# Kernel optimization log

Hardware: AMD Instinct MI355X
Metric: run time of the kernel (lower is better)

Reference implementation:

```python
import jax, jax.numpy as jnp
import numpy as np

KERNEL_SIZE = 9
B, C, H, W = 8, 32, 512, 512


def setup_inputs() -> dict:
    key = jax.random.key(0)
    image = jax.random.uniform(key, (B, C, H, W), dtype=jnp.float32)
    return {"image": image}


def _make_kernels(channels, k, dtype):
    # kernel1: point-select (identity) depthwise kernel
    k1 = jnp.zeros((channels, 1, k, k), dtype=dtype).at[:, 0, k // 2, k // 2].set(1.0)
    # kernel2: all -2, center = k*k - 2
    k2 = jnp.full((channels, 1, k, k), -2.0, dtype=dtype).at[:, 0, k // 2, k // 2].set(float(k * k - 2))
    # kernel3: ones box filter
    k3 = jnp.ones((channels, 1, k, k), dtype=dtype)
    return k1, k2, k3


def _dwconv(x, ker, channels, k):
    pad = k // 2  # 'same' padding for odd k
    return jax.lax.conv_general_dilated(
        x, ker,
        window_strides=(1, 1),
        padding=[(pad, pad), (pad, pad)],
        dimension_numbers=("NCHW", "OIHW", "NCHW"),
        feature_group_count=channels,
    )


def reference(image):
    channels = image.shape[1]
    k = KERNEL_SIZE
    k1, k2, k3 = _make_kernels(channels, k, image.dtype)
    im_sq = jnp.square(image)
    conv1 = _dwconv(image, k1, channels, k)   # identity point-select
    conv2 = _dwconv(image, k2, channels, k)   # box(-2) with center correction
    conv3 = _dwconv(im_sq, k3, channels, k)   # box sum of squares
    convsum = conv1 * conv2 + conv3
    # sum over (C,H,W) per batch element, then mean over batch
    return jnp.mean(jnp.sum(convsum, axis=(1, 2, 3)))
```

## Files before the change

kernel.cpp:

```cpp
#include <hip/hip_runtime.h>

#define HH 512
#define WW 512
#define SEGS 16
#define SEGROWS 32
#define CG 128

__device__ __forceinline__ int imax(int a, int b) { return a > b ? a : b; }
__device__ __forceinline__ int imin(int a, int b) { return a < b ? a : b; }

__global__ __launch_bounds__(256, 4) void scc_kernel(const float* __restrict__ img,
                                                     float* __restrict__ out) {
    const int tid   = blockIdx.x * 256 + threadIdx.x;
    const int g     = tid & (CG - 1);
    const int rest  = tid >> 7;
    const int seg   = rest & (SEGS - 1);
    const int plane = rest >> 4;

    const float* base = img + (size_t)plane * (HH * WW);
    const int r0 = seg * SEGROWS;

    float4 cw;
    {
        int w0 = 4 * g;
        cw.x = (float)(9 - imax(0, 4 - (w0 + 0)) - imax(0, (w0 + 0) - (WW - 5)));
        cw.y = (float)(9 - imax(0, 4 - (w0 + 1)) - imax(0, (w0 + 1) - (WW - 5)));
        cw.z = (float)(9 - imax(0, 4 - (w0 + 2)) - imax(0, (w0 + 2) - (WW - 5)));
        cw.w = (float)(9 - imax(0, 4 - (w0 + 3)) - imax(0, (w0 + 3) - (WW - 5)));
    }

    const int offL = imax(g - 1, 0) * 16;
    const int offC = g * 16;
    const int offR = imin(g + 1, CG - 1) * 16;
    const float mL = (g > 0) ? 1.f : 0.f;
    const float mR = (g < CG - 1) ? 1.f : 0.f;

    const float4 z4 = make_float4(0.f, 0.f, 0.f, 0.f);
    float4 x0 = z4, x1 = z4, x2 = z4, x3 = z4, x4 = z4,
           x5 = z4, x6 = z4, x7 = z4, x8 = z4;
    float4 q0 = z4, q1 = z4, q2 = z4, q3 = z4, q4 = z4;
    float4 V = z4;
    float accW = 0.f, accRV = 0.f;

#pragma unroll 8
    for (int i = 0; i < SEGROWS + 8; ++i) {
        const int r  = r0 - 4 + i;
        const int rc_ = imin(imax(r, 0), HH - 1);
        const float m = ((unsigned)r < (unsigned)HH) ? 1.f : 0.f;
        const char* rowb = (const char*)(base + (ptrdiff_t)rc_ * WW);

        float4 lcr = *(const float4*)(rowb + offL);
        float4 ccr = *(const float4*)(rowb + offC);
        float4 rcr = *(const float4*)(rowb + offR);

        const float a = mL * m, b = mR * m;
        float4 lc = make_float4(lcr.x * a, lcr.y * a, lcr.z * a, lcr.w * a);
        float4 cc = make_float4(ccr.x * m, ccr.y * m, ccr.z * m, ccr.w * m);
        float4 rc = make_float4(rcr.x * b, rcr.y * b, rcr.z * b, rcr.w * b);

        float R0 = ((lc.x + lc.y) + (lc.z + lc.w)) + ((cc.x + cc.y) + (cc.z + cc.w)) + rc.x;
        float R1 = R0 - lc.x + rc.y;
        float R2 = R1 - lc.y + rc.z;
        float R3 = R2 - lc.z + rc.w;
        float4 Rn = make_float4(R0, R1, R2, R3);

        V.x += cc.x - x0.x;  V.y += cc.y - x0.y;
        V.z += cc.z - x0.z;  V.w += cc.w - x0.w;

        x0 = x1; x1 = x2; x2 = x3; x3 = x4; x4 = x5;
        x5 = x6; x6 = x7; x7 = x8; x8 = cc;
        q0 = q1; q1 = q2; q2 = q3; q3 = q4; q4 = Rn;

        if (i >= 8) {
            const int h = r - 4;
            const float chf = (float)(9 - imax(0, 4 - h) - imax(0, h - (HH - 5)));
            float w0 = fmaf(chf, cw.x, 81.f);
            float w1 = fmaf(chf, cw.y, 81.f);
            float w2 = fmaf(chf, cw.z, 81.f);
            float w3 = fmaf(chf, cw.w, 81.f);
            accW = fmaf(w0 * x4.x, x4.x, accW);
            accW = fmaf(w1 * x4.y, x4.y, accW);
            accW = fmaf(w2 * x4.z, x4.z, accW);
            accW = fmaf(w3 * x4.w, x4.w, accW);
            accRV = fmaf(q0.x, V.x, accRV);
            accRV = fmaf(q0.y, V.y, accRV);
            accRV = fmaf(q0.z, V.z, accRV);
            accRV = fmaf(q0.w, V.w, accRV);
        }
    }

    float acc = accW - 2.f * accRV;

#pragma unroll
    for (int off = 32; off > 0; off >>= 1)
        acc += __shfl_xor(acc, off, 64);
    __shared__ float wsum[4];
    const int lane = threadIdx.x & 63;
    const int wv   = threadIdx.x >> 6;
    if (lane == 0) wsum[wv] = acc;
    __syncthreads();
    if (threadIdx.x == 0) {
        float s = (wsum[0] + wsum[1]) + (wsum[2] + wsum[3]);
        atomicAdd(out, 0.125f * s);
    }
}

extern "C" void kernel_launch(void* const* d_in, const int* in_sizes, int n_in,
                              void* d_out, int out_size, void* d_ws, size_t ws_size,
                              hipStream_t stream) {
    const float* img = (const float*)d_in[0];
    float* out = (float*)d_out;
    hipMemsetAsync(out, 0, sizeof(float), stream);
    scc_kernel<<<dim3(2048), dim3(256), 0, stream>>>(img, out);
}
```

Measured before the change: 371.5 us.

## Double segment height, halve grid, swizzle block order, peel warm-up rows

Each thread now streams 64 output rows instead of 32, which halves the grid to 1024 blocks and cuts the redundant 8-row halo reads per segment. Block indices are swizzled so consecutive blocks land on different planes and segments, to spread memory traffic across channels and XCDs. The 8-row warm-up is peeled into a separate unrolled loop, which removes the per-iteration i>=8 branch from the main loop. The trade-off is fewer resident waves on a device with many CUs, which may reduce latency hiding.

```diff
diff --git a/kernel.cpp b/kernel.cpp
--- a/kernel.cpp
+++ b/kernel.cpp
@@ -2,20 +2,50 @@
 
 #define HH 512
 #define WW 512
-#define SEGS 16
-#define SEGROWS 32
+#define SEGS 8
+#define LOG2SEGS 3
+#define SEGROWS 64
 #define CG 128
+#define NBLOCKS 1024
 
 __device__ __forceinline__ int imax(int a, int b) { return a > b ? a : b; }
 __device__ __forceinline__ int imin(int a, int b) { return a < b ? a : b; }
 
+
+#define STREAM_ROW(rr)                                                         \
+    {                                                                          \
+        const int r   = (rr);                                                  \
+        const int rc_ = imin(imax(r, 0), HH - 1);                              \
+        const float m = ((unsigned)r < (unsigned)HH) ? 1.f : 0.f;              \
+        const char* rowb = (const char*)(base + (ptrdiff_t)rc_ * WW);          \
+        float4 lcr = *(const float4*)(rowb + offL);                            \
+        float4 ccr = *(const float4*)(rowb + offC);                            \
+        float4 rcr = *(const float4*)(rowb + offR);                            \
+        const float a = mL * m, b = mR * m;                                    \
+        float4 lc = make_float4(lcr.x * a, lcr.y * a, lcr.z * a, lcr.w * a);   \
+        float4 cc = make_float4(ccr.x * m, ccr.y * m, ccr.z * m, ccr.w * m);   \
+        float4 rc = make_float4(rcr.x * b, rcr.y * b, rcr.z * b, rcr.w * b);   \
+        float R0 = ((lc.x + lc.y) + (lc.z + lc.w)) +                           \
+                   ((cc.x + cc.y) + (cc.z + cc.w)) + rc.x;                     \
+        float R1 = R0 - lc.x + rc.y;                                           \
+        float R2 = R1 - lc.y + rc.z;                                           \
+        float R3 = R2 - lc.z + rc.w;                                           \
+        float4 Rn = make_float4(R0, R1, R2, R3);                               \
+        V.x += cc.x - x0.x; V.y += cc.y - x0.y;                                \
+        V.z += cc.z - x0.z; V.w += cc.w - x0.w;                                \
+        x0 = x1; x1 = x2; x2 = x3; x3 = x4; x4 = x5;                           \
+        x5 = x6; x6 = x7; x7 = x8; x8 = cc;                                    \
+        q0 = q1; q1 = q2; q2 = q3; q3 = q4; q4 = Rn;                           \
+    }
+
 __global__ __launch_bounds__(256, 4) void scc_kernel(const float* __restrict__ img,
                                                      float* __restrict__ out) {
-    const int tid   = blockIdx.x * 256 + threadIdx.x;
+    const int swz   = (blockIdx.x & 7) * (NBLOCKS / 8) + (blockIdx.x >> 3);
+    const int tid   = swz * 256 + (int)threadIdx.x;
     const int g     = tid & (CG - 1);
     const int rest  = tid >> 7;
     const int seg   = rest & (SEGS - 1);
-    const int plane = rest >> 4;
+    const int plane = rest >> LOG2SEGS;
 
     const float* base = img + (size_t)plane * (HH * WW);
     const int r0 = seg * SEGROWS;
@@ -42,51 +72,28 @@
     float4 V = z4;
     float accW = 0.f, accRV = 0.f;
 
+#pragma unroll
+    for (int i = 0; i < 8; ++i) {
+        STREAM_ROW(r0 - 4 + i)
+    }
+
 #pragma unroll 8
-    for (int i = 0; i < SEGROWS + 8; ++i) {
-        const int r  = r0 - 4 + i;
-        const int rc_ = imin(imax(r, 0), HH - 1);
-        const float m = ((unsigned)r < (unsigned)HH) ? 1.f : 0.f;
-        const char* rowb = (const char*)(base + (ptrdiff_t)rc_ * WW);
-
-        float4 lcr = *(const float4*)(rowb + offL);
-        float4 ccr = *(const float4*)(rowb + offC);
-        float4 rcr = *(const float4*)(rowb + offR);
-
-        const float a = mL * m, b = mR * m;
-        float4 lc = make_float4(lcr.x * a, lcr.y * a, lcr.z * a, lcr.w * a);
-        float4 cc = make_float4(ccr.x * m, ccr.y * m, ccr.z * m, ccr.w * m);
-        float4 rc = make_float4(rcr.x * b, rcr.y * b, rcr.z * b, rcr.w * b);
-
-        float R0 = ((lc.x + lc.y) + (lc.z + lc.w)) + ((cc.x + cc.y) + (cc.z + cc.w)) + rc.x;
-        float R1 = R0 - lc.x + rc.y;
-        float R2 = R1 - lc.y + rc.z;
-        float R3 = R2 - lc.z + rc.w;
-        float4 Rn = make_float4(R0, R1, R2, R3);
-
-        V.x += cc.x - x0.x;  V.y += cc.y - x0.y;
-        V.z += cc.z - x0.z;  V.w += cc.w - x0.w;
-
-        x0 = x1; x1 = x2; x2 = x3; x3 = x4; x4 = x5;
-        x5 = x6; x6 = x7; x7 = x8; x8 = cc;
-        q0 = q1; q1 = q2; q2 = q3; q3 = q4; q4 = Rn;
-
-        if (i >= 8) {
-            const int h = r - 4;
-            const float chf = (float)(9 - imax(0, 4 - h) - imax(0, h - (HH - 5)));
-            float w0 = fmaf(chf, cw.x, 81.f);
-            float w1 = fmaf(chf, cw.y, 81.f);
-            float w2 = fmaf(chf, cw.z, 81.f);
-            float w3 = fmaf(chf, cw.w, 81.f);
-            accW = fmaf(w0 * x4.x, x4.x, accW);
-            accW = fmaf(w1 * x4.y, x4.y, accW);
-            accW = fmaf(w2 * x4.z, x4.z, accW);
-            accW = fmaf(w3 * x4.w, x4.w, accW);
-            accRV = fmaf(q0.x, V.x, accRV);
-            accRV = fmaf(q0.y, V.y, accRV);
-            accRV = fmaf(q0.z, V.z, accRV);
-            accRV = fmaf(q0.w, V.w, accRV);
-        }
+    for (int i = 8; i < SEGROWS + 8; ++i) {
+        STREAM_ROW(r0 - 4 + i)
+        const int h = r0 + i - 8;
+        const float chf = (float)(9 - imax(0, 4 - h) - imax(0, h - (HH - 5)));
+        float w0 = fmaf(chf, cw.x, 81.f);
+        float w1 = fmaf(chf, cw.y, 81.f);
+        float w2 = fmaf(chf, cw.z, 81.f);
+        float w3 = fmaf(chf, cw.w, 81.f);
+        accW = fmaf(w0 * x4.x, x4.x, accW);
+        accW = fmaf(w1 * x4.y, x4.y, accW);
+        accW = fmaf(w2 * x4.z, x4.z, accW);
+        accW = fmaf(w3 * x4.w, x4.w, accW);
+        accRV = fmaf(q0.x, V.x, accRV);
+        accRV = fmaf(q0.y, V.y, accRV);
+        accRV = fmaf(q0.z, V.z, accRV);
+        accRV = fmaf(q0.w, V.w, accRV);
     }
 
     float acc = accW - 2.f * accRV;
@@ -111,5 +118,5 @@
     const float* img = (const float*)d_in[0];
     float* out = (float*)d_out;
     hipMemsetAsync(out, 0, sizeof(float), stream);
-    scc_kernel<<<dim3(2048), dim3(256), 0, stream>>>(img, out);
+    scc_kernel<<<dim3(NBLOCKS), dim3(256), 0, stream>>>(img, out);
 }
```

New measurement: 389.2 us. 4.8% more time.
